# Kernel tuning notes

Measured on AMD Instinct MI355X. Metric: run time of the kernel, lower is better.

## Reference

```python
import jax, jax.numpy as jnp
import numpy as np

D_MODEL, N_HEADS, D_FF = 768, 12, 3072
D_HEAD = D_MODEL // N_HEADS
EPS = 1e-5


def layer_norm(x, g, b):
    mu = jnp.mean(x, axis=-1, keepdims=True)
    var = jnp.mean(jnp.square(x - mu), axis=-1, keepdims=True)
    return (x - mu) * jax.lax.rsqrt(var + EPS) * g + b


def setup_inputs() -> dict:
    key = jax.random.key(0)
    ks = jax.random.split(key, 8)
    B, T = 4, 2048
    s_in = 1.0 / np.sqrt(D_MODEL)
    s_ff = 1.0 / np.sqrt(D_FF)
    return {
        "x": jax.random.normal(ks[0], (B, T, D_MODEL), dtype=jnp.float32),
        "ln1_g": jnp.ones((D_MODEL,), jnp.float32),
        "ln1_b": jnp.zeros((D_MODEL,), jnp.float32),
        "qkv_w": jax.random.normal(ks[1], (D_MODEL, 3 * D_MODEL), jnp.float32) * s_in,
        "qkv_b": jnp.zeros((3 * D_MODEL,), jnp.float32),
        "attn_out_w": jax.random.normal(ks[2], (D_MODEL, D_MODEL), jnp.float32) * s_in,
        "attn_out_b": jnp.zeros((D_MODEL,), jnp.float32),
        "ln2_g": jnp.ones((D_MODEL,), jnp.float32),
        "ln2_b": jnp.zeros((D_MODEL,), jnp.float32),
        "ff1_w": jax.random.normal(ks[3], (D_MODEL, D_FF), jnp.float32) * s_in,
        "ff1_b": jnp.zeros((D_FF,), jnp.float32),
        "ff2_w": jax.random.normal(ks[4], (D_FF, D_MODEL), jnp.float32) * s_ff,
        "ff2_b": jnp.zeros((D_MODEL,), jnp.float32),
    }


def reference(x, ln1_g, ln1_b, qkv_w, qkv_b, attn_out_w, attn_out_b,
              ln2_g, ln2_b, ff1_w, ff1_b, ff2_w, ff2_b):
    B, T, D = x.shape
    h = layer_norm(x, ln1_g, ln1_b)
    qkv = h @ qkv_w + qkv_b                       # [B,T,3D]
    q, k, v = jnp.split(qkv, 3, axis=-1)
    def heads(t):  # [B,T,D] -> [B,H,T,dh]
        return t.reshape(B, T, N_HEADS, D_HEAD).transpose(0, 2, 1, 3)
    q, k, v = heads(q), heads(k), heads(v)
    scores = jnp.einsum('bhqd,bhkd->bhqk', q, k) / np.sqrt(D_HEAD)
    attn = jnp.einsum('bhqk,bhkd->bhqd', jax.nn.softmax(scores, axis=-1), v)
    attn = attn.transpose(0, 2, 1, 3).reshape(B, T, D)
    x = x + attn @ attn_out_w + attn_out_b
    h = layer_norm(x, ln2_g, ln2_b)
    ff = jax.nn.gelu(h @ ff1_w + ff1_b, approximate=True) @ ff2_w + ff2_b
    return x + ff
```

## Files before the change

### kernel.cpp

```cpp
#include <hip/hip_runtime.h>
#include <stdint.h>

typedef unsigned short ushort_t;
typedef unsigned int uint_t;

typedef __bf16 bf16x8 __attribute__((ext_vector_type(8)));
typedef float f32x4 __attribute__((ext_vector_type(4)));

#define DM 768
#define DFF 3072
#define NH 12
#define DH 64
#define TLEN 2048
#define BATCH 4
#define NROWS (BATCH * TLEN)
#define QKVW (3 * DM)
#define STG ((size_t)NROWS * DM)

#if __has_builtin(__builtin_amdgcn_exp2f)
#define EXP2(x) __builtin_amdgcn_exp2f(x)
#else
extern "C" __device__ float __ocml_native_exp2_f32(float);
#define EXP2(x) __ocml_native_exp2_f32(x)
#endif

__device__ __forceinline__ float b2f(ushort_t u) {
  union { uint_t i; float f; } c; c.i = ((uint_t)u) << 16; return c.f;
}
__device__ __forceinline__ ushort_t f2b(float f) {
  union { float f; uint_t i; } c; c.f = f;
  uint_t i = c.i;
  return (ushort_t)((i + 0x7fffu + ((i >> 16) & 1u)) >> 16);
}

__device__ __forceinline__ void gl_lds16(const ushort_t* g, ushort_t* l) {
  __builtin_amdgcn_global_load_lds(
      (const __attribute__((address_space(1))) uint_t*)g,
      (__attribute__((address_space(3))) uint_t*)l, 16, 0, 0);
}

__device__ __forceinline__ float gelu_f(float x) {
  float x2 = x * x;
  float c2n = -x * __builtin_fmaf(0.10294323f, x2, 2.3022082f);
  float t = EXP2(c2n);
  return x * __builtin_amdgcn_rcpf(1.0f + t);
}

__global__ __launch_bounds__(256) void detect_dtype(const ushort_t* __restrict__ x,
                                                    int* __restrict__ flag) {
  __shared__ int cnt[256];
  int c = 0;
  for (int i = threadIdx.x; i < 65536; i += 256)
    c += ((x[i] & 0x7F80u) == 0x7F80u) ? 1 : 0;
  cnt[threadIdx.x] = c;
  __syncthreads();
  for (int s = 128; s >= 1; s >>= 1) {
    if (threadIdx.x < s) cnt[threadIdx.x] += cnt[threadIdx.x + s];
    __syncthreads();
  }
  if (threadIdx.x == 0) flag[0] = (cnt[0] > 0) ? 1 : 0;
}

__global__ __launch_bounds__(256) void cvt_smalls(
    const void* s0, const void* s1, const void* s2, const void* s3,
    const void* s4, const void* s5, const void* s6, const void* s7,
    ushort_t* __restrict__ dst, const int* __restrict__ flag) {
  int f = flag[0];
  int i = blockIdx.x * 256 + threadIdx.x;
  if (i >= 9984) return;
  const void* src; int off;
  if (i < 768)       { src = s0; off = i; }
  else if (i < 1536) { src = s1; off = i - 768; }
  else if (i < 3840) { src = s2; off = i - 1536; }
  else if (i < 4608) { src = s3; off = i - 3840; }
  else if (i < 5376) { src = s4; off = i - 4608; }
  else if (i < 6144) { src = s5; off = i - 5376; }
  else if (i < 9216) { src = s6; off = i - 6144; }
  else               { src = s7; off = i - 9216; }
  dst[i] = f ? f2b(((const float*)src)[off]) : ((const ushort_t*)src)[off];
}

__global__ __launch_bounds__(256) void transpose_adapt(
    const void* __restrict__ inbase, long long inOff, ushort_t* __restrict__ out,
    int R, int C, int ldIn, const int* __restrict__ flag) {
  __shared__ alignas(16) ushort_t tile[32][33];
  int f = flag[0];
  const float* in32 = (const float*)inbase + inOff;
  const ushort_t* in16 = (const ushort_t*)inbase + inOff;
  int tc = blockIdx.x * 32, tr = blockIdx.y * 32;
  int lx = threadIdx.x & 31, ly = threadIdx.x >> 5;
#pragma unroll
  for (int i = 0; i < 32; i += 8) {
    size_t idx = (size_t)(tr + ly + i) * ldIn + tc + lx;
    tile[ly + i][lx] = f ? f2b(in32[idx]) : in16[idx];
  }
  __syncthreads();
#pragma unroll
  for (int i = 0; i < 32; i += 8)
    out[(size_t)(tc + ly + i) * R + tr + lx] = tile[lx][ly + i];
}

template <bool RAW>
__global__ __launch_bounds__(256) void ln_kernel(
    const void* __restrict__ xr, const ushort_t* __restrict__ g,
    const ushort_t* __restrict__ b, ushort_t* __restrict__ out,
    const int* __restrict__ flag) {
  int row = blockIdx.x * 4 + (threadIdx.x >> 6);
  int lane = threadIdx.x & 63;
  float v[12];
  if (RAW && flag[0]) {
    const float2* xp = (const float2*)((const float*)xr + (size_t)row * DM);
#pragma unroll
    for (int j = 0; j < 6; j++) {
      float2 t = xp[lane + 64 * j];
      v[2 * j] = t.x; v[2 * j + 1] = t.y;
    }
  } else {
    const uint_t* xu = (const uint_t*)((const ushort_t*)xr + (size_t)row * DM);
#pragma unroll
    for (int j = 0; j < 6; j++) {
      uint_t wv = xu[lane + 64 * j];
      v[2 * j] = b2f((ushort_t)(wv & 0xffffu));
      v[2 * j + 1] = b2f((ushort_t)(wv >> 16));
    }
  }
  float sum = 0.f, ss = 0.f;
#pragma unroll
  for (int k = 0; k < 12; k++) { sum += v[k]; ss += v[k] * v[k]; }
#pragma unroll
  for (int off = 32; off >= 1; off >>= 1) {
    sum += __shfl_xor(sum, off, 64);
    ss += __shfl_xor(ss, off, 64);
  }
  float mu = sum * (1.f / DM);
  float var = ss * (1.f / DM) - mu * mu;
  float rs = rsqrtf(var + 1e-5f);
  uint_t* ou = (uint_t*)(out + (size_t)row * DM);
  const uint_t* gu = (const uint_t*)g;
  const uint_t* bu = (const uint_t*)b;
#pragma unroll
  for (int j = 0; j < 6; j++) {
    int idx = lane + 64 * j;
    uint_t gw = gu[idx], bw = bu[idx];
    float o0 = (v[2 * j] - mu) * rs * b2f((ushort_t)(gw & 0xffffu)) + b2f((ushort_t)(bw & 0xffffu));
    float o1 = (v[2 * j + 1] - mu) * rs * b2f((ushort_t)(gw >> 16)) + b2f((ushort_t)(bw >> 16));
    ou[idx] = (uint_t)f2b(o0) | ((uint_t)f2b(o1) << 16);
  }
}

template <bool GELU, int RESMODE, int OUTMODE, int BM = 128>
__global__ __launch_bounds__(256) void gemm_bt(
    const ushort_t* __restrict__ A, const ushort_t* __restrict__ BT,
    const ushort_t* __restrict__ bias, const void* __restrict__ res,
    void* __restrict__ outp, int M, int N, int K, int accum,
    const int* __restrict__ flagp) {
  constexpr int MI = (BM == 128) ? 4 : 2;
  constexpr int NI = 4;
  __shared__ alignas(16) ushort_t sA[BM * 32];
  __shared__ alignas(16) ushort_t sB[128 * 32];
  const int m0 = blockIdx.x * BM;
  const int n0 = blockIdx.y * 128;
  const int tid = threadIdx.x;
  const int w = tid >> 6, lane = tid & 63;
  const int quad = lane >> 4, l16 = lane & 15;
  const int wm = (w & 1) * (BM / 2);
  const int wn = (w >> 1) * 64;

  const f32x4 vz = {0.f, 0.f, 0.f, 0.f};
  f32x4 acc[MI][NI];
#pragma unroll
  for (int i = 0; i < MI; i++)
#pragma unroll
    for (int j = 0; j < NI; j++) acc[i][j] = vz;

  const int colA = (lane & 3) * 8;
  const int rowAa = w * (BM / 4) + (lane >> 2);
  const int rowBb = w * 32 + (lane >> 2);
  const ushort_t* gA = A + (size_t)(m0 + rowAa) * K + colA;
  const ushort_t* gB = BT + (size_t)(n0 + rowBb) * K + colA;
  ushort_t* lA = &sA[(w * (BM / 4)) * 32];
  ushort_t* lB = &sB[(w * 32) * 32];

  for (int k0 = 0; k0 < K; k0 += 32) {
    gl_lds16(gA + k0, lA);
    if constexpr (BM == 128) gl_lds16(gA + k0 + (size_t)16 * K, lA + 16 * 32);
    gl_lds16(gB + k0, lB);
    gl_lds16(gB + k0 + (size_t)16 * K, lB + 16 * 32);
    __syncthreads();
    bf16x8 af[MI], bfr[NI];
#pragma unroll
    for (int i = 0; i < MI; i++)
      af[i] = *(const bf16x8*)&sA[(wm + i * 16 + l16) * 32 + quad * 8];
#pragma unroll
    for (int i = 0; i < NI; i++)
      bfr[i] = *(const bf16x8*)&sB[(wn + i * 16 + l16) * 32 + quad * 8];
#pragma unroll
    for (int mi = 0; mi < MI; mi++)
#pragma unroll
      for (int ni = 0; ni < NI; ni++)
        acc[mi][ni] = __builtin_amdgcn_mfma_f32_16x16x32_bf16(af[mi], bfr[ni], acc[mi][ni], 0, 0, 0);
    __syncthreads();
  }

  ushort_t* o16 = (ushort_t*)outp;
  float* o32 = (float*)outp;
  const int f32io = (OUTMODE == 1 || RESMODE == 2) ? flagp[0] : 0;
#pragma unroll
  for (int mi = 0; mi < MI; mi++) {
#pragma unroll
    for (int ni = 0; ni < NI; ni++) {
      int col = n0 + wn + ni * 16 + l16;
      float bs = bias ? b2f(bias[col]) : 0.0f;
#pragma unroll
      for (int r = 0; r < 4; r++) {
        int row = m0 + wm + mi * 16 + quad * 4 + r;
        size_t idx = (size_t)row * N + col;
        float v = acc[mi][ni][r] + bs;
        if (GELU) v = gelu_f(v);
        if (RESMODE == 1) v += b2f(((const ushort_t*)res)[idx]);
        if (RESMODE == 2)
          v += f32io ? ((const float*)res)[idx] : b2f(((const ushort_t*)res)[idx]);
        if (OUTMODE == 1) {
          if (accum) v += f32io ? o32[idx] : b2f(o16[idx]);
          if (f32io) o32[idx] = v; else o16[idx] = f2b(v);
        } else if (OUTMODE == 2) {
          int b = row >> 11, kt = (row >> 7) & 15, kl = row & 127;
          int ty = col >= 1536 ? 2 : (col >= 768 ? 1 : 0);
          int c2 = col - ty * 768;
          int hh = c2 >> 6, d = c2 & 63;
          if (ty == 0) v *= 0.18033688011112042f;
          size_t tb = ((size_t)(b * NH + hh) * 16 + kt) * 8192;
          size_t sidx;
          if (ty == 2) {
            int pl = (kl & 0x60) | ((kl & 15) << 1) | ((kl >> 4) & 1);
            sidx = tb + (size_t)d * 128 + (size_t)(((pl >> 3) ^ (d & 7)) << 3) + (pl & 7);
          } else {
            sidx = tb + (size_t)kl * 64 + (size_t)(((d >> 3) ^ (kl & 7)) << 3) + (d & 7);
          }
          o16[ty * STG + sidx] = f2b(v);
        } else {
          o16[idx] = f2b(v);
        }
      }
    }
  }
}

__global__ __launch_bounds__(256) void attn_kernel(
    const ushort_t* __restrict__ qs, const ushort_t* __restrict__ ks,
    const ushort_t* __restrict__ vs, ushort_t* __restrict__ attnout) {
  __shared__ alignas(16) ushort_t sK[2][64 * 64];
  __shared__ alignas(16) ushort_t sV[2][64 * 64];
  __shared__ alignas(16) ushort_t sP[4 * 2 * 32 * 40];
  const int bh = blockIdx.x;
  const int qt = blockIdx.y;
  const int tid = threadIdx.x;
  const int w = tid >> 6, lane = tid & 63;
  const int quad = lane >> 4, l16 = lane & 15;
  const int xsw = l16 & 7;
  const ushort_t* ktg0 = ks + (size_t)bh * 16 * 8192;
  const ushort_t* vtg0 = vs + (size_t)bh * 16 * 8192;

  {
    const ushort_t* qtg = qs + ((size_t)bh * 16 + qt) * 8192;
#pragma unroll
    for (int i = 0; i < 4; i++) {
      int off = (w * 4 + i) * 512;
      ushort_t* dst = (off < 4096) ? &sK[0][off] : &sK[1][off - 4096];
      gl_lds16(qtg + off + lane * 8, dst);
    }
  }
  __syncthreads();
  bf16x8 qf[2][2];
#pragma unroll
  for (int mq = 0; mq < 2; mq++) {
    int q = w * 32 + mq * 16 + l16;
    const ushort_t* sq = (q < 64) ? &sK[0][q * 64] : &sK[1][(q - 64) * 64];
#pragma unroll
    for (int c = 0; c < 2; c++)
      qf[mq][c] = *(const bf16x8*)&sq[((c * 4 + quad) ^ (q & 7)) * 8];
  }
  __syncthreads();

  bf16x8 onesf;
#pragma unroll
  for (int i = 0; i < 8; i++) onesf[i] = (__bf16)1.0f;

  f32x4 lsum[2];
  f32x4 oacc[2][4];
  const f32x4 vz = {0.f, 0.f, 0.f, 0.f};
#pragma unroll
  for (int mq = 0; mq < 2; mq++) {
    lsum[mq] = vz;
#pragma unroll
    for (int nd = 0; nd < 4; nd++) oacc[mq][nd] = vz;
  }

  auto stage = [&](int j, int buf) {
    const ushort_t* kg = ktg0 + (size_t)(j >> 1) * 8192 + (j & 1) * 4096;
    const ushort_t* vg = vtg0 + (size_t)(j >> 1) * 8192 + (j & 1) * 64;
#pragma unroll
    for (int i = 0; i < 2; i++) {
      int off = (w * 2 + i) * 512;
      gl_lds16(kg + off + lane * 8, &sK[buf][off]);
      gl_lds16(vg + (size_t)((w * 2 + i) * 8 + (lane >> 3)) * 128 + (lane & 7) * 8,
               &sV[buf][off]);
    }
  };

  stage(0, 0);

  for (int j = 0; j < 32; j++) {
    const int buf = j & 1;
    __syncthreads();
    if (j < 31) stage(j + 1, 1 - buf);

    f32x4 s[2][4];
    __builtin_amdgcn_s_setprio(1);
#pragma unroll
    for (int nk = 0; nk < 4; nk++) {
      int key = nk * 16 + l16;
      bf16x8 kf0 = *(const bf16x8*)&sK[buf][key * 64 + ((quad) ^ (key & 7)) * 8];
      bf16x8 kf1 = *(const bf16x8*)&sK[buf][key * 64 + ((4 + quad) ^ (key & 7)) * 8];
#pragma unroll
      for (int mq = 0; mq < 2; mq++) {
        s[mq][nk] = __builtin_amdgcn_mfma_f32_16x16x32_bf16(qf[mq][0], kf0, vz, 0, 0, 0);
        s[mq][nk] = __builtin_amdgcn_mfma_f32_16x16x32_bf16(qf[mq][1], kf1, s[mq][nk], 0, 0, 0);
      }
    }
    __builtin_amdgcn_s_setprio(0);

    uint_t* myP32 = (uint_t*)sP + w * 1280;
#pragma unroll
    for (int kk = 0; kk < 2; kk++)
#pragma unroll
      for (int mq = 0; mq < 2; mq++)
#pragma unroll
        for (int r = 0; r < 4; r++) {
          float lo = EXP2(s[mq][kk * 2 + 0][r]);
          float hi = EXP2(s[mq][kk * 2 + 1][r]);
          uint_t pk;
          asm("v_cvt_pk_bf16_f32 %0, %1, %2" : "=v"(pk) : "v"(lo), "v"(hi));
          myP32[kk * 640 + (mq * 16 + quad * 4 + r) * 20 + l16] = pk;
        }
    __asm__ volatile("s_waitcnt lgkmcnt(0)" ::: "memory");

    bf16x8 pf[2][2];
#pragma unroll
    for (int kk = 0; kk < 2; kk++)
#pragma unroll
      for (int mq = 0; mq < 2; mq++)
        pf[kk][mq] = *(const bf16x8*)&sP[(size_t)w * 2560 + kk * 1280 +
                                         (mq * 16 + l16) * 40 + quad * 8];
    __builtin_amdgcn_s_setprio(1);
#pragma unroll
    for (int kk = 0; kk < 2; kk++)
#pragma unroll
      for (int mq = 0; mq < 2; mq++)
        lsum[mq] = __builtin_amdgcn_mfma_f32_16x16x32_bf16(pf[kk][mq], onesf, lsum[mq], 0, 0, 0);
#pragma unroll
    for (int kk = 0; kk < 2; kk++)
#pragma unroll
      for (int nd = 0; nd < 4; nd++) {
        bf16x8 vf = *(const bf16x8*)&sV[buf][(nd * 16 + l16) * 64 + ((kk * 4 + quad) ^ xsw) * 8];
#pragma unroll
        for (int mq = 0; mq < 2; mq++)
          oacc[mq][nd] = __builtin_amdgcn_mfma_f32_16x16x32_bf16(pf[kk][mq], vf, oacc[mq][nd], 0, 0, 0);
      }
    __builtin_amdgcn_s_setprio(0);
    __asm__ volatile("" ::: "memory");
  }

  const int b = bh / NH, h = bh - b * NH;
#pragma unroll
  for (int mq = 0; mq < 2; mq++) {
    float inv[4];
#pragma unroll
    for (int r = 0; r < 4; r++) inv[r] = __builtin_amdgcn_rcpf(lsum[mq][r]);
#pragma unroll
    for (int nd = 0; nd < 4; nd++) {
#pragma unroll
      for (int r = 0; r < 4; r++) {
        size_t row = (size_t)b * TLEN + qt * 128 + w * 32 + mq * 16 + quad * 4 + r;
        int col = h * DH + nd * 16 + l16;
        attnout[row * DM + col] = f2b(oacc[mq][nd][r] * inv[r]);
      }
    }
  }
}

extern "C" void kernel_launch(void* const* d_in, const int* in_sizes, int n_in,
                              void* d_out, int out_size, void* d_ws, size_t ws_size,
                              hipStream_t stream) {
  const void* x_r = d_in[0];
  const void* ln1_g_r = d_in[1];
  const void* ln1_b_r = d_in[2];
  const void* qkv_w_r = d_in[3];
  const void* qkv_b_r = d_in[4];
  const void* ao_w_r = d_in[5];
  const void* ao_b_r = d_in[6];
  const void* ln2_g_r = d_in[7];
  const void* ln2_b_r = d_in[8];
  const void* ff1_w_r = d_in[9];
  const void* ff1_b_r = d_in[10];
  const void* ff2_w_r = d_in[11];
  const void* ff2_b_r = d_in[12];

  int* flag = (int*)d_ws;
  ushort_t* base = (ushort_t*)d_ws + 128;
  const size_t RD = STG;

  const size_t elA = RD + RD + (size_t)NROWS * DFF + RD + (size_t)DM * DM + 9984;
  const bool pathA = ws_size >= elA * 2 + 4096;

  detect_dtype<<<1, 256, 0, stream>>>((const ushort_t*)x_r, flag);

  if (pathA) {
    ushort_t* x2   = base;
    ushort_t* h    = base + RD;
    ushort_t* big  = base + 2 * RD;
    ushort_t* aux  = big + (size_t)NROWS * DFF;
    ushort_t* wTa  = aux + RD;
    ushort_t* smalls = wTa + (size_t)DM * DM;
    ushort_t* wTq = aux;
    ushort_t* attnb = aux;
    ushort_t* wT2 = aux;
    ushort_t* wT3 = aux + (size_t)DFF * DM;
    ushort_t *g1 = smalls, *b1 = smalls + 768, *qb = smalls + 1536, *ab = smalls + 3840,
             *g2 = smalls + 4608, *b2 = smalls + 5376, *f1b = smalls + 6144, *f2bb = smalls + 9216;

    cvt_smalls<<<39, 256, 0, stream>>>(ln1_g_r, ln1_b_r, qkv_b_r, ao_b_r,
                                       ln2_g_r, ln2_b_r, ff1_b_r, ff2_b_r, smalls, flag);
    ln_kernel<true><<<NROWS / 4, 256, 0, stream>>>(x_r, g1, b1, h, flag);
    transpose_adapt<<<dim3(QKVW / 32, DM / 32), 256, 0, stream>>>(qkv_w_r, 0, wTq, DM, QKVW, QKVW, flag);
    gemm_bt<false, 0, 2><<<dim3(NROWS / 128, QKVW / 128), 256, 0, stream>>>(
        h, wTq, qb, nullptr, big, NROWS, QKVW, DM, 0, flag);
    attn_kernel<<<dim3(NH * BATCH, 16), 256, 0, stream>>>(big, big + STG, big + 2 * STG, attnb);
    transpose_adapt<<<dim3(DM / 32, DM / 32), 256, 0, stream>>>(ao_w_r, 0, wTa, DM, DM, DM, flag);
    gemm_bt<false, 2, 0, 64><<<dim3(NROWS / 64, DM / 128), 256, 0, stream>>>(
        attnb, wTa, ab, x_r, x2, NROWS, DM, DM, 0, flag);
    ln_kernel<false><<<NROWS / 4, 256, 0, stream>>>(x2, g2, b2, h, flag);
    transpose_adapt<<<dim3(DFF / 32, DM / 32), 256, 0, stream>>>(ff1_w_r, 0, wT2, DM, DFF, DFF, flag);
    gemm_bt<true, 0, 0><<<dim3(NROWS / 128, DFF / 128), 256, 0, stream>>>(
        h, wT2, f1b, nullptr, big, NROWS, DFF, DM, 0, flag);
    transpose_adapt<<<dim3(DM / 32, DFF / 32), 256, 0, stream>>>(ff2_w_r, 0, wT3, DFF, DM, DM, flag);
    gemm_bt<false, 1, 1, 64><<<dim3(NROWS / 64, DM / 128), 256, 0, stream>>>(
        big, wT3, f2bb, x2, d_out, NROWS, DM, DFF, 0, flag);
  } else {
    ushort_t* regA = base;
    ushort_t* regB = base + RD;
    ushort_t* slots = regB + (size_t)NROWS * QKVW;
    ushort_t* smalls = slots + (size_t)QKVW * DM + (size_t)DM * DM;
    ushort_t* h = regA, *attnb = regA, *h2 = regA;
    ushort_t* x2 = regB;
    ushort_t* ffq = regB + RD;
    ushort_t* wTq = slots;
    ushort_t* wTa = slots + (size_t)QKVW * DM;
    ushort_t* wT2 = slots;
    ushort_t* wT3 = slots + (size_t)1536 * DM;
    ushort_t *g1 = smalls, *b1 = smalls + 768, *qb = smalls + 1536, *ab = smalls + 3840,
             *g2 = smalls + 4608, *b2 = smalls + 5376, *f1b = smalls + 6144, *f2bb = smalls + 9216;

    cvt_smalls<<<39, 256, 0, stream>>>(ln1_g_r, ln1_b_r, qkv_b_r, ao_b_r,
                                       ln2_g_r, ln2_b_r, ff1_b_r, ff2_b_r, smalls, flag);
    ln_kernel<true><<<NROWS / 4, 256, 0, stream>>>(x_r, g1, b1, h, flag);
    transpose_adapt<<<dim3(QKVW / 32, DM / 32), 256, 0, stream>>>(qkv_w_r, 0, wTq, DM, QKVW, QKVW, flag);
    gemm_bt<false, 0, 2><<<dim3(NROWS / 128, QKVW / 128), 256, 0, stream>>>(
        h, wTq, qb, nullptr, regB, NROWS, QKVW, DM, 0, flag);
    attn_kernel<<<dim3(NH * BATCH, 16), 256, 0, stream>>>(regB, regB + STG, regB + 2 * STG, attnb);
    transpose_adapt<<<dim3(DM / 32, DM / 32), 256, 0, stream>>>(ao_w_r, 0, wTa, DM, DM, DM, flag);
    gemm_bt<false, 2, 0, 64><<<dim3(NROWS / 64, DM / 128), 256, 0, stream>>>(
        attnb, wTa, ab, x_r, x2, NROWS, DM, DM, 0, flag);
    ln_kernel<false><<<NROWS / 4, 256, 0, stream>>>(x2, g2, b2, h2, flag);
    for (int q = 0; q < 2; q++) {
      transpose_adapt<<<dim3(1536 / 32, DM / 32), 256, 0, stream>>>(
          ff1_w_r, (long long)q * 1536, wT2, DM, 1536, DFF, flag);
      gemm_bt<true, 0, 0><<<dim3(NROWS / 128, 1536 / 128), 256, 0, stream>>>(
          h2, wT2, f1b + q * 1536, nullptr, ffq, NROWS, 1536, DM, 0, flag);
      transpose_adapt<<<dim3(DM / 32, 1536 / 32), 256, 0, stream>>>(
          ff2_w_r, (long long)q * 1536 * DM, wT3, 1536, DM, DM, flag);
      if (q == 0)
        gemm_bt<false, 1, 1, 64><<<dim3(NROWS / 64, DM / 128), 256, 0, stream>>>(
            ffq, wT3, f2bb, x2, d_out, NROWS, DM, 1536, 0, flag);
      else
        gemm_bt<false, 0, 1, 64><<<dim3(NROWS / 64, DM / 128), 256, 0, stream>>>(
            ffq, wT3, nullptr, nullptr, d_out, NROWS, DM, 1536, 1, flag);
    }
  }
}
```

Measured before the change: 470.5 us.

## Double-buffer GEMM LDS tiles and swizzle K-chunks to avoid bank conflicts

The bf16 MFMA GEMM now keeps two LDS buffers per operand. It issues the global-to-LDS load for the next K-slice before computing on the current one, so fetch latency overlaps the MFMAs and one barrier per iteration is removed. It also rotates each row's 8-element K-chunk position by a row-dependent offset on store and undoes it on read, to spread LDS bank accesses for the fragment loads. This doubles the shared-memory footprint, which may reduce occupancy.

```diff
diff --git a/kernel.cpp b/kernel.cpp
--- a/kernel.cpp
+++ b/kernel.cpp
@@ -156,8 +156,8 @@
     const int* __restrict__ flagp) {
   constexpr int MI = (BM == 128) ? 4 : 2;
   constexpr int NI = 4;
-  __shared__ alignas(16) ushort_t sA[BM * 32];
-  __shared__ alignas(16) ushort_t sB[128 * 32];
+  __shared__ alignas(16) ushort_t sA[2][BM * 32];
+  __shared__ alignas(16) ushort_t sB[2][128 * 32];
   const int m0 = blockIdx.x * BM;
   const int n0 = blockIdx.y * 128;
   const int tid = threadIdx.x;
@@ -173,27 +173,40 @@
 #pragma unroll
     for (int j = 0; j < NI; j++) acc[i][j] = vz;
 
-  const int colA = (lane & 3) * 8;
+  const int colA = (((lane & 3) + ((lane >> 3) & 3)) & 3) * 8;
   const int rowAa = w * (BM / 4) + (lane >> 2);
   const int rowBb = w * 32 + (lane >> 2);
   const ushort_t* gA = A + (size_t)(m0 + rowAa) * K + colA;
   const ushort_t* gB = BT + (size_t)(n0 + rowBb) * K + colA;
-  ushort_t* lA = &sA[(w * (BM / 4)) * 32];
-  ushort_t* lB = &sB[(w * 32) * 32];
-
-  for (int k0 = 0; k0 < K; k0 += 32) {
+
+  auto stage = [&](int k0, int buf) {
+    ushort_t* lA = &sA[buf][(w * (BM / 4)) * 32];
+    ushort_t* lB = &sB[buf][(w * 32) * 32];
     gl_lds16(gA + k0, lA);
     if constexpr (BM == 128) gl_lds16(gA + k0 + (size_t)16 * K, lA + 16 * 32);
     gl_lds16(gB + k0, lB);
     gl_lds16(gB + k0 + (size_t)16 * K, lB + 16 * 32);
-    __syncthreads();
+  };
+
+  stage(0, 0);
+  __syncthreads();
+
+  const int nk = K >> 5;
+  for (int kt = 0; kt < nk; ++kt) {
+    const int buf = kt & 1;
+    if (kt + 1 < nk) stage((kt + 1) << 5, 1 - buf);
+
     bf16x8 af[MI], bfr[NI];
 #pragma unroll
-    for (int i = 0; i < MI; i++)
-      af[i] = *(const bf16x8*)&sA[(wm + i * 16 + l16) * 32 + quad * 8];
-#pragma unroll
-    for (int i = 0; i < NI; i++)
-      bfr[i] = *(const bf16x8*)&sB[(wn + i * 16 + l16) * 32 + quad * 8];
+    for (int i = 0; i < MI; i++) {
+      int ra = wm + i * 16 + l16;
+      af[i] = *(const bf16x8*)&sA[buf][ra * 32 + ((quad + 4 - ((ra >> 1) & 3)) & 3) * 8];
+    }
+#pragma unroll
+    for (int i = 0; i < NI; i++) {
+      int rb = wn + i * 16 + l16;
+      bfr[i] = *(const bf16x8*)&sB[buf][rb * 32 + ((quad + 4 - ((rb >> 1) & 3)) & 3) * 8];
+    }
 #pragma unroll
     for (int mi = 0; mi < MI; mi++)
 #pragma unroll
@@ -224,12 +237,12 @@
           if (accum) v += f32io ? o32[idx] : b2f(o16[idx]);
           if (f32io) o32[idx] = v; else o16[idx] = f2b(v);
         } else if (OUTMODE == 2) {
-          int b = row >> 11, kt = (row >> 7) & 15, kl = row & 127;
+          int b = row >> 11, kt2 = (row >> 7) & 15, kl = row & 127;
           int ty = col >= 1536 ? 2 : (col >= 768 ? 1 : 0);
           int c2 = col - ty * 768;
           int hh = c2 >> 6, d = c2 & 63;
           if (ty == 0) v *= 0.18033688011112042f;
-          size_t tb = ((size_t)(b * NH + hh) * 16 + kt) * 8192;
+          size_t tb = ((size_t)(b * NH + hh) * 16 + kt2) * 8192;
           size_t sidx;
           if (ty == 2) {
             int pl = (kl & 0x60) | ((kl & 15) << 1) | ((kl >> 4) & 1);
```

After: 482.8 us. +2.6%, slower.
